# Kernel tuning notes

Hardware: AMD Instinct MI355X
Metric: run time of the kernel (lower is better)

## Reference

```python
import jax, jax.numpy as jnp
import numpy as np

BS, QLEN, KLEN = 2, 64, 64
N_HEADS, D_KV = 8, 64
INNER = N_HEADS * D_KV  # 512
VOCAB = 4096


def _layernorm(x, g, b, eps=1e-6):
    m = jnp.mean(x, axis=-1, keepdims=True)
    v = jnp.mean(jnp.square(x - m), axis=-1, keepdims=True)
    return (x - m) * jax.lax.rsqrt(v + eps) * g + b


def _l2norm(x, eps=1e-12):
    sq = jnp.sum(jnp.square(x), axis=-1, keepdims=True)
    return x * jax.lax.rsqrt(jnp.maximum(sq, eps))


def setup_inputs() -> dict:
    key = jax.random.key(0)
    ks = jax.random.split(key, 8)
    d = {
        'query': jax.random.normal(ks[0], (BS, QLEN, INNER), jnp.float32),
        'key': jax.random.normal(ks[1], (BS, KLEN, INNER), jnp.float32),
        'q_position_embeddings': jax.random.normal(ks[2], (BS, QLEN, INNER), jnp.float32),
        'k_position_embeddings': jax.random.normal(ks[3], (BS, KLEN, INNER), jnp.float32),
        'wi_w': jax.random.normal(ks[4], (2 * INNER, INNER), jnp.float32) / np.sqrt(2 * INNER),
        'vq_dict': jax.random.normal(ks[5], (VOCAB, D_KV), jnp.float32) * np.sqrt(2.0 / (VOCAB + D_KV)),
        'vq_ln_g': jnp.ones((D_KV,), jnp.float32),
        'vq_ln_b': jnp.zeros((D_KV,), jnp.float32),
        'vq_o_w': jax.random.normal(ks[6], (D_KV, D_KV), jnp.float32) / np.sqrt(D_KV),
        'ln_g': jnp.ones((D_KV,), jnp.float32),
        'ln_b': jnp.zeros((D_KV,), jnp.float32),
    }
    return d


def reference(query, key, q_position_embeddings, k_position_embeddings,
              wi_w, vq_dict, vq_ln_g, vq_ln_b, vq_o_w, ln_g, ln_b):
    bs, qlen, dim = query.shape
    klen = key.shape[1]

    q = query + q_position_embeddings
    k = key + k_position_embeddings
    # wi(concat([q, 0])) == q @ wi_w[:dim]; wi(concat([0, k])) == k @ wi_w[dim:]
    q_proj = jnp.einsum('bqd,de->bqe', q, wi_w[:dim])   # [bs, qlen, inner]
    k_proj = jnp.einsum('bkd,de->bke', k, wi_w[dim:])   # [bs, klen, inner]

    # pairwise outer sum -> [bs, qlen, klen, inner] -> tokens of size d_kv
    rcr = q_proj[:, :, None, :] + k_proj[:, None, :, :]
    y = rcr.reshape(bs, qlen * klen * N_HEADS, D_KV)

    # --- VectorQuantizer (eval mode: no dropout, loss = 0) ---
    y_n = _l2norm(y)
    d_n = _l2norm(vq_dict)
    sim = jnp.einsum('bnd,vd->bnv', y_n, d_n)           # [bs, N, vocab]
    word_idx = jnp.argmax(sim, axis=-1)                 # [bs, N] int
    word_sim = jnp.max(sim, axis=-1)                    # [bs, N]
    z = vq_dict[word_idx]                               # gather
    emb = jax.lax.stop_gradient(z - y) + y              # straight-through
    emb = _layernorm(emb, vq_ln_g, vq_ln_b)
    emb = jnp.einsum('bnd,de->bne', emb, vq_o_w)

    r3 = emb.reshape(bs, qlen, klen, N_HEADS, D_KV)
    r3_scores = word_sim.reshape(bs, qlen, klen, N_HEADS, 1)
    out_ids = word_idx.reshape(bs, qlen, klen, N_HEADS, 1)

    r3_weighted = jnp.mean(r3 * r3_scores, axis=2)      # [bs, qlen, n_heads, d_kv]
    r3_weighted = jnp.transpose(r3_weighted, (0, 2, 1, 3))  # [bs, n_heads, qlen, d_kv]
    r3_weighted = _layernorm(r3_weighted, ln_g, ln_b)
    return r3_weighted, out_ids, r3_scores
```

## Files before the change

### kernel.cpp

```cpp
#include <hip/hip_runtime.h>
#include <math.h>

#define BS 2
#define QLEN 64
#define KLEN 64
#define NH 8
#define DKV 64
#define INNER 512
#define VOCAB 4096
#define CHUNKV 64
#define RS 130
#define BUFD (CHUNKV * RS)

typedef double vdbl4 __attribute__((ext_vector_type(4)));
typedef double vdbl2 __attribute__((ext_vector_type(2)));


__global__ __launch_bounds__(256) void k_prep(
    const float* __restrict__ q_in, const float* __restrict__ k_in,
    const float* __restrict__ qpe, const float* __restrict__ kpe,
    const float* __restrict__ wi,
    const float* __restrict__ vq, const float* __restrict__ g,
    const float* __restrict__ bta, const float* __restrict__ ow,
    double* __restrict__ qp, double* __restrict__ kp,
    double* __restrict__ dnt, float* __restrict__ E,
    unsigned long long* __restrict__ bestf)
{
    __shared__ double S[1600];
    __shared__ float Osh[4096];
    int bid = blockIdx.x;
    int t = threadIdx.x;

    if (bid < 1024) {
        int side = bid >> 9;
        int b    = (bid >> 8) & 1;
        int rp   = (bid >> 3) & 31;
        int cb   = bid & 7;
        const float* xin = side ? k_in : q_in;
        const float* pin = side ? kpe : qpe;
        double* outp = side ? kp : qp;
        int wrow0 = side ? INNER : 0;
        int r0 = rp * 2;
        double* xs = S;
        double* red = S + 1024;
        for (int i = t; i < 2 * INNER; i += 256) {
            int rr = i >> 9, dd = i & 511;
            int gidx = (b * 64 + r0 + rr) * INNER + dd;
            xs[rr * INNER + dd] = (double)xin[gidx] + (double)pin[gidx];
        }
        __syncthreads();
        int col = cb * 64 + (t & 63);
        int dh = t >> 6;
        double a0 = 0.0, a1 = 0.0;
        #pragma unroll 8
        for (int d = dh * 128; d < dh * 128 + 128; ++d) {
            double w = (double)wi[(size_t)(wrow0 + d) * INNER + col];
            a0 = fma(xs[d], w, a0);
            a1 = fma(xs[INNER + d], w, a1);
        }
        red[(dh * 2 + 0) * 64 + (t & 63)] = a0;
        red[(dh * 2 + 1) * 64 + (t & 63)] = a1;
        __syncthreads();
        if (t < 128) {
            int rr = t >> 6, c2 = t & 63;
            double s = (red[(0 * 2 + rr) * 64 + c2] + red[(1 * 2 + rr) * 64 + c2])
                     + (red[(2 * 2 + rr) * 64 + c2] + red[(3 * 2 + rr) * 64 + c2]);
            outp[(size_t)(b * 64 + r0 + rr) * INNER + cb * 64 + c2] = s;
        }
    } else {
        int db = bid - 1024;
        if (db < 256) bestf[db * 256 + t] = 0ull;
        double* Lsh = S;
        double* Dsh = S + 256;
        int vb = db * 4;
        int wv = t >> 6, lane = t & 63;
        for (int i = t; i < 4096; i += 256) Osh[i] = ow[i];
        int v = vb + wv;
        double z = (double)vq[v * DKV + lane];
        double s2 = z * z, s1 = z;
        for (int m = 32; m >= 1; m >>= 1) { s2 += __shfl_xor(s2, m); s1 += __shfl_xor(s1, m); }
        Dsh[lane * 5 + wv] = z * (1.0 / sqrt(fmax(s2, 1e-12)));
        double mean = s1 * (1.0 / 64.0);
        double d0 = z - mean;
        double vv2 = d0 * d0;
        for (int m = 32; m >= 1; m >>= 1) vv2 += __shfl_xor(vv2, m);
        vv2 *= (1.0 / 64.0);
        Lsh[wv * 64 + lane] = d0 * (1.0 / sqrt(vv2 + 1e-6)) * (double)g[lane] + (double)bta[lane];
        __syncthreads();
        double c0 = 0.0, c1 = 0.0, c2 = 0.0, c3 = 0.0;
        #pragma unroll 4
        for (int gg = 0; gg < 16; ++gg) {
            int jj = gg * 4;
            c0 = fma(Lsh[wv * 64 + jj + 0], (double)Osh[(jj + 0) * 64 + lane], c0);
            c1 = fma(Lsh[wv * 64 + jj + 1], (double)Osh[(jj + 1) * 64 + lane], c1);
            c2 = fma(Lsh[wv * 64 + jj + 2], (double)Osh[(jj + 2) * 64 + lane], c2);
            c3 = fma(Lsh[wv * 64 + jj + 3], (double)Osh[(jj + 3) * 64 + lane], c3);
        }
        E[v * DKV + lane] = (float)((c0 + c1) + (c2 + c3));
        {
            int j = t >> 2, vloc = t & 3;
            dnt[(size_t)j * VOCAB + vb + vloc] = Dsh[j * 5 + vloc];
        }
    }
}

__global__ __launch_bounds__(1024, 4) void k_simscan(
    const double* __restrict__ qp, const double* __restrict__ kp,
    const double* __restrict__ dnt,
    unsigned long long* __restrict__ bestf)
{
    int bid = blockIdx.x;
    int bh = bid & 15, cg = bid >> 4;
    int b = bh >> 3, h = bh & 7;
    int t = threadIdx.x;
    int w = t >> 6, l = t & 63;

    __shared__ double S[2 * BUFD];
    __shared__ int sem[8];

    int asub = l >> 4;
    int lrow = l & 15;
    bool isprod = (w < 8);

    if (t < 8) sem[t] = 0;

    int drow[4], dcol[4];
    {
        vdbl4 prow = (vdbl4){0.0, 0.0, 0.0, 0.0};
        vdbl4 pcol = (vdbl4){0.0, 0.0, 0.0, 0.0};
        double a_row = (asub == 0) ? (double)lrow : 0.0;
        double b_one = (asub == 0) ? 1.0 : 0.0;
        double a_one = (asub == 0) ? 1.0 : 0.0;
        double b_col = (asub == 0) ? (double)lrow : 0.0;
        prow = __builtin_amdgcn_mfma_f64_16x16x4f64(a_row, b_one, prow, 0, 0, 0);
        pcol = __builtin_amdgcn_mfma_f64_16x16x4f64(a_one, b_col, pcol, 0, 0, 0);
        #pragma unroll
        for (int r = 0; r < 4; ++r) { drow[r] = (int)prow[r]; dcol[r] = (int)pcol[r]; }
    }

    double afr[16];
    if (isprod) {
        const double* src = (w < 4) ? qp : kp;
        int arow = (w & 3) * 16 + lrow;
        #pragma unroll
        for (int ks = 0; ks < 16; ++ks)
            afr[ks] = src[(size_t)(b * 64 + arow) * INNER + h * 64 + ks * 4 + asub];
    }

    int ci = t - 512;
    int qg = ci & 15, kg = (ci >> 4) & 31;
    double best[4][2];
    #pragma unroll
    for (int i = 0; i < 4; ++i)
        #pragma unroll
        for (int j = 0; j < 2; ++j) best[i][j] = 0.0;

    __syncthreads();

    if (isprod) {
        for (int step = 0; step < 4; ++step) {
            if (step >= 2) {
                for (;;) {
                    int c0 = 0;
                    if (l == 0) c0 = atomicAdd(&sem[4 + step - 2], 0);
                    if (__shfl(c0, 0) >= 8) break;
                    __builtin_amdgcn_s_sleep(2);
                }
            }
            int v0 = (cg * 4 + step) * CHUNKV;
            double* buf = S + (step & 1) * BUFD;
            vdbl4 acc[4];
            #pragma unroll
            for (int vt = 0; vt < 4; ++vt) acc[vt] = (vdbl4){0.0, 0.0, 0.0, 0.0};
            size_t base = (size_t)asub * VOCAB + v0 + lrow;
            double bcur[4], bnext[4];
            #pragma unroll
            for (int vt = 0; vt < 4; ++vt) bcur[vt] = dnt[base + vt * 16];
            #pragma unroll
            for (int ks = 0; ks < 16; ++ks) {
                if (ks < 15) {
                    size_t krow = base + (size_t)((ks + 1) * 4) * VOCAB;
                    #pragma unroll
                    for (int vt = 0; vt < 4; ++vt) bnext[vt] = dnt[krow + vt * 16];
                }
                #pragma unroll
                for (int vt = 0; vt < 4; ++vt)
                    acc[vt] = __builtin_amdgcn_mfma_f64_16x16x4f64(
                        afr[ks], bcur[vt], acc[vt], 0, 0, 0);
                if (ks < 15) {
                    #pragma unroll
                    for (int vt = 0; vt < 4; ++vt) bcur[vt] = bnext[vt];
                }
            }
            bool isq = (w < 4);
            #pragma unroll
            for (int vt = 0; vt < 4; ++vt)
                #pragma unroll
                for (int r = 0; r < 4; ++r) {
                    int vl = vt * 16 + dcol[r];
                    int grow = (w & 3) * 16 + drow[r];
                    int slot = isq ? ((grow & 15) * 4 + (grow >> 4))
                                   : (64 + (grow & 31) * 2 + (grow >> 5));
                    unsigned long long code =
                        (unsigned long long)((4095 - (v0 + vl)) << 1);
                    double s = fma(acc[vt][r], 1.0 / 64.0, 1.5);
                    unsigned long long bb2 = __double_as_longlong(s) & ~0x1FFFull;
                    if (isq) bb2 |= code;
                    buf[vl * RS + slot] = __longlong_as_double(bb2);
                }
            __threadfence_block();
            if (l == 0) atomicAdd(&sem[step], 1);
        }
    } else {
        for (int step = 0; step < 4; ++step) {
            for (;;) {
                int c0 = 0;
                if (l == 0) c0 = atomicAdd(&sem[step], 0);
                if (__shfl(c0, 0) >= 8) break;
                __builtin_amdgcn_s_sleep(2);
            }
            double* buf = S + (step & 1) * BUFD;
            #pragma unroll 2
            for (int v = 0; v < CHUNKV; ++v) {
                vdbl2 q01 = *(const vdbl2*)&buf[v * RS + qg * 4];
                vdbl2 q23 = *(const vdbl2*)&buf[v * RS + qg * 4 + 2];
                vdbl2 k01 = *(const vdbl2*)&buf[v * RS + 64 + kg * 2];
                best[0][0] = fmax(best[0][0], q01[0] + k01[0]);
                best[0][1] = fmax(best[0][1], q01[0] + k01[1]);
                best[1][0] = fmax(best[1][0], q01[1] + k01[0]);
                best[1][1] = fmax(best[1][1], q01[1] + k01[1]);
                best[2][0] = fmax(best[2][0], q23[0] + k01[0]);
                best[2][1] = fmax(best[2][1], q23[0] + k01[1]);
                best[3][0] = fmax(best[3][0], q23[1] + k01[0]);
                best[3][1] = fmax(best[3][1], q23[1] + k01[1]);
            }
            __threadfence_block();
            if (l == 0) atomicAdd(&sem[4 + step], 1);
        }
        #pragma unroll
        for (int i = 0; i < 4; ++i)
            #pragma unroll
            for (int j = 0; j < 2; ++j) {
                int q = qg + 16 * i, k = kg + 32 * j;
                atomicMax(&bestf[((size_t)bh * 64 + q) * 64 + k],
                          (unsigned long long)__double_as_longlong(best[i][j]));
            }
    }
}

__global__ __launch_bounds__(256) void k_combine(
    const unsigned long long* __restrict__ bestf,
    const double* __restrict__ qp, const double* __restrict__ kp,
    const float* __restrict__ E,
    const float* __restrict__ lng, const float* __restrict__ lnb,
    float* __restrict__ out)
{
    int bid = blockIdx.x;
    int bh = bid & 15, q = bid >> 4;
    int b = bh >> 3, h = bh & 7;
    int t = threadIdx.x;
    int w = t >> 6, lane = t & 63;

    __shared__ double qrow[64];
    __shared__ double gpart[4][64];
    __shared__ double knpart[4][64];
    __shared__ double qnpart[4];
    __shared__ float  ws_l[64];
    __shared__ int    idx_l[64];
    __shared__ float  epart[4][64];

    if (t < 64) qrow[t] = qp[(size_t)(b * 64 + q) * INNER + h * 64 + t];
    __syncthreads();

    {
        const double* krow = kp + (size_t)(b * 64 + lane) * INNER + h * 64 + w * 16;
        double gd = 0.0, kn = 0.0;
        #pragma unroll
        for (int i = 0; i < 16; ++i) {
            double xk = krow[i];
            gd = fma(qrow[w * 16 + i], xk, gd);
            kn = fma(xk, xk, kn);
        }
        gpart[w][lane] = gd;
        knpart[w][lane] = kn;
        if (lane == 0) {
            double qn = 0.0;
            #pragma unroll
            for (int i = 0; i < 16; ++i) { double xq = qrow[w * 16 + i]; qn = fma(xq, xq, qn); }
            qnpart[w] = qn;
        }
    }
    __syncthreads();

    if (w == 0) {
        int k = lane;
        double gdot = (gpart[0][k] + gpart[1][k]) + (gpart[2][k] + gpart[3][k]);
        double kn2  = (knpart[0][k] + knpart[1][k]) + (knpart[2][k] + knpart[3][k]);
        double qn2  = (qnpart[0] + qnpart[1]) + (qnpart[2] + qnpart[3]);
        unsigned long long bb = bestf[((size_t)bh * 64 + q) * 64 + k];
        int vidx = 4095 - (int)(bb & 0xFFFull);
        double sval = __longlong_as_double(bb & ~0x1FFFull);
        double tru = (sval - 3.0) * 64.0;
        double n2 = qn2 + kn2 + 2.0 * gdot;
        double wsim = tru * (1.0 / sqrt(fmax(n2, 1e-12)));
        size_t oidx = ((size_t)(b * QLEN + q) * KLEN + k) * NH + h;
        out[65536 + oidx] = (float)vidx;
        out[131072 + oidx] = (float)wsim;
        ws_l[k] = (float)wsim;
        idx_l[k] = vidx;
    }
    __syncthreads();

    {
        int d = lane;
        float acc = 0.0f;
        #pragma unroll 4
        for (int k2 = w * 16; k2 < w * 16 + 16; ++k2)
            acc += E[idx_l[k2] * DKV + d] * ws_l[k2];
        epart[w][d] = acc;
    }
    __syncthreads();

    if (w == 0) {
        int d = lane;
        float acc = ((epart[0][d] + epart[1][d]) + (epart[2][d] + epart[3][d])) * (1.0f / 64.0f);
        float mean = acc;
        for (int m = 32; m >= 1; m >>= 1) mean += __shfl_xor(mean, m);
        mean *= (1.0f / 64.0f);
        float dv = acc - mean;
        float var = dv * dv;
        for (int m = 32; m >= 1; m >>= 1) var += __shfl_xor(var, m);
        var *= (1.0f / 64.0f);
        float o = dv * rsqrtf(var + 1e-6f) * lng[d] + lnb[d];
        out[(((size_t)b * NH + h) * QLEN + q) * DKV + d] = o;
    }
}

extern "C" void kernel_launch(void* const* d_in, const int* in_sizes, int n_in,
                              void* d_out, int out_size, void* d_ws, size_t ws_size,
                              hipStream_t stream) {
    const float* query = (const float*)d_in[0];
    const float* key   = (const float*)d_in[1];
    const float* qpe   = (const float*)d_in[2];
    const float* kpe   = (const float*)d_in[3];
    const float* wi    = (const float*)d_in[4];
    const float* vq    = (const float*)d_in[5];
    const float* vqg   = (const float*)d_in[6];
    const float* vqb   = (const float*)d_in[7];
    const float* ow    = (const float*)d_in[8];
    const float* lng   = (const float*)d_in[9];
    const float* lnb   = (const float*)d_in[10];
    float* out = (float*)d_out;

    char* ws = (char*)d_ws;
    double* qp  = (double*)(ws + 0);
    double* kp  = (double*)(ws + 524288);
    double* dnt = (double*)(ws + 1048576);
    float*  E   = (float*) (ws + 3145728);
    unsigned long long* bestf = (unsigned long long*)(ws + 4194304);

    k_prep   <<<2048, 256, 0, stream>>>(query, key, qpe, kpe, wi, vq, vqg, vqb, ow,
                                        qp, kp, dnt, E, bestf);
    k_simscan<<<256, 1024, 0, stream>>>(qp, kp, dnt, bestf);
    k_combine<<<1024, 256, 0, stream>>>(bestf, qp, kp, E, lng, lnb, out);
}
```

Before: 153.5 us.

## Use FP64 MFMA for projection GEMM in prep kernel with larger tiles

Rewrites the q/k projection part of k_prep to use 16x16x4 FP64 MFMA instructions on 16-row tiles with a split-K reduction through shared memory, instead of scalar FMA over two rows per block. The dictionary-preparation branch is regrouped to handle 8 vocab entries per 512-thread block, and the launch shrinks from 2048 to 768 blocks. This cuts redundant weight reads and scalar FP64 work in the prep stage. The cost is a large shared-memory footprint (about 128 KB) that may limit occupancy, plus an MFMA trick used to derive the output lane layout.

```diff
diff --git a/kernel.cpp b/kernel.cpp
--- a/kernel.cpp
+++ b/kernel.cpp
@@ -11,12 +11,13 @@
 #define CHUNKV 64
 #define RS 130
 #define BUFD (CHUNKV * RS)
+#define XSTR 514
 
 typedef double vdbl4 __attribute__((ext_vector_type(4)));
 typedef double vdbl2 __attribute__((ext_vector_type(2)));
 
 
-__global__ __launch_bounds__(256) void k_prep(
+__global__ __launch_bounds__(512) void k_prep(
     const float* __restrict__ q_in, const float* __restrict__ k_in,
     const float* __restrict__ qpe, const float* __restrict__ kpe,
     const float* __restrict__ wi,
@@ -26,60 +27,93 @@
     double* __restrict__ dnt, float* __restrict__ E,
     unsigned long long* __restrict__ bestf)
 {
-    __shared__ double S[1600];
-    __shared__ float Osh[4096];
+    __shared__ double S[16448];
     int bid = blockIdx.x;
     int t = threadIdx.x;
-
-    if (bid < 1024) {
-        int side = bid >> 9;
-        int b    = (bid >> 8) & 1;
-        int rp   = (bid >> 3) & 31;
-        int cb   = bid & 7;
+    int w = t >> 6, l = t & 63;
+    int lrow = l & 15, asub = l >> 4;
+
+    if (bid < 256) {
+        int rt = bid >> 4, cg = bid & 15;
+        int side = rt >> 3;
         const float* xin = side ? k_in : q_in;
         const float* pin = side ? kpe : qpe;
         double* outp = side ? kp : qp;
         int wrow0 = side ? INNER : 0;
-        int r0 = rp * 2;
         double* xs = S;
-        double* red = S + 1024;
-        for (int i = t; i < 2 * INNER; i += 256) {
-            int rr = i >> 9, dd = i & 511;
-            int gidx = (b * 64 + r0 + rr) * INNER + dd;
-            xs[rr * INNER + dd] = (double)xin[gidx] + (double)pin[gidx];
+        double* red = S + 8224;
+
+        int drow[4], dcol[4];
+        {
+            vdbl4 prow = (vdbl4){0.0, 0.0, 0.0, 0.0};
+            vdbl4 pcol = (vdbl4){0.0, 0.0, 0.0, 0.0};
+            double a_row = (asub == 0) ? (double)lrow : 0.0;
+            double b_one = (asub == 0) ? 1.0 : 0.0;
+            double a_one = (asub == 0) ? 1.0 : 0.0;
+            double b_col = (asub == 0) ? (double)lrow : 0.0;
+            prow = __builtin_amdgcn_mfma_f64_16x16x4f64(a_row, b_one, prow, 0, 0, 0);
+            pcol = __builtin_amdgcn_mfma_f64_16x16x4f64(a_one, b_col, pcol, 0, 0, 0);
+            #pragma unroll
+            for (int r = 0; r < 4; ++r) { drow[r] = (int)prow[r]; dcol[r] = (int)pcol[r]; }
+        }
+
+        for (int i = t; i < 16 * 512; i += 512) {
+            int r = i >> 9, d = i & 511;
+            int grow = rt * 16 + r;
+            int b = (grow >> 6) & 1, row = grow & 63;
+            int gg = (b * 64 + row) * INNER + d;
+            xs[r * XSTR + d] = (double)xin[gg] + (double)pin[gg];
         }
         __syncthreads();
-        int col = cb * 64 + (t & 63);
-        int dh = t >> 6;
-        double a0 = 0.0, a1 = 0.0;
-        #pragma unroll 8
-        for (int d = dh * 128; d < dh * 128 + 128; ++d) {
-            double w = (double)wi[(size_t)(wrow0 + d) * INNER + col];
-            a0 = fma(xs[d], w, a0);
-            a1 = fma(xs[INNER + d], w, a1);
-        }
-        red[(dh * 2 + 0) * 64 + (t & 63)] = a0;
-        red[(dh * 2 + 1) * 64 + (t & 63)] = a1;
+
+        int cq = w & 1, kq = w >> 1;
+        int colb = cg * 32 + cq * 16;
+        int k0 = kq * 128;
+        vdbl4 acc = (vdbl4){0.0, 0.0, 0.0, 0.0};
+        double bf[2];
+        #pragma unroll
+        for (int p = 0; p < 2; ++p)
+            bf[p] = (double)wi[(size_t)(wrow0 + k0 + p * 4 + asub) * INNER + colb + lrow];
+        #pragma unroll 4
+        for (int ks = 0; ks < 32; ++ks) {
+            double a = xs[lrow * XSTR + k0 + ks * 4 + asub];
+            double bc = bf[ks & 1];
+            if (ks < 30)
+                bf[ks & 1] = (double)wi[(size_t)(wrow0 + k0 + (ks + 2) * 4 + asub) * INNER
+                                        + colb + lrow];
+            acc = __builtin_amdgcn_mfma_f64_16x16x4f64(a, bc, acc, 0, 0, 0);
+        }
+        {
+            double* rr = red + (size_t)(cq * 4 + kq) * 1028;
+            #pragma unroll
+            for (int r = 0; r < 4; ++r) rr[l * 4 + r] = acc[r];
+        }
         __syncthreads();
-        if (t < 128) {
-            int rr = t >> 6, c2 = t & 63;
-            double s = (red[(0 * 2 + rr) * 64 + c2] + red[(1 * 2 + rr) * 64 + c2])
-                     + (red[(2 * 2 + rr) * 64 + c2] + red[(3 * 2 + rr) * 64 + c2]);
-            outp[(size_t)(b * 64 + r0 + rr) * INNER + cb * 64 + c2] = s;
+        if (kq == 0) {
+            #pragma unroll
+            for (int r = 0; r < 4; ++r) {
+                int base = l * 4 + r;
+                double s0 = red[(cq * 4 + 0) * 1028 + base] + red[(cq * 4 + 1) * 1028 + base];
+                double s1 = red[(cq * 4 + 2) * 1028 + base] + red[(cq * 4 + 3) * 1028 + base];
+                int grow = rt * 16 + drow[r];
+                int b = (grow >> 6) & 1, row = grow & 63;
+                outp[(size_t)(b * 64 + row) * INNER + colb + dcol[r]] = s0 + s1;
+            }
         }
     } else {
-        int db = bid - 1024;
-        if (db < 256) bestf[db * 256 + t] = 0ull;
+        int db = bid - 256;
+        if (t < 128) bestf[db * 128 + t] = 0ull;
         double* Lsh = S;
-        double* Dsh = S + 256;
-        int vb = db * 4;
-        int wv = t >> 6, lane = t & 63;
-        for (int i = t; i < 4096; i += 256) Osh[i] = ow[i];
+        double* Dsh = S + 512;
+        float*  Osh = (float*)(S + 1088);
+        int vb = db * 8;
+        int wv = w, lane = l;
+        for (int i = t; i < 4096; i += 512) Osh[i] = ow[i];
         int v = vb + wv;
         double z = (double)vq[v * DKV + lane];
         double s2 = z * z, s1 = z;
         for (int m = 32; m >= 1; m >>= 1) { s2 += __shfl_xor(s2, m); s1 += __shfl_xor(s1, m); }
-        Dsh[lane * 5 + wv] = z * (1.0 / sqrt(fmax(s2, 1e-12)));
+        Dsh[lane * 9 + wv] = z * (1.0 / sqrt(fmax(s2, 1e-12)));
         double mean = s1 * (1.0 / 64.0);
         double d0 = z - mean;
         double vv2 = d0 * d0;
@@ -98,8 +132,8 @@
         }
         E[v * DKV + lane] = (float)((c0 + c1) + (c2 + c3));
         {
-            int j = t >> 2, vloc = t & 3;
-            dnt[(size_t)j * VOCAB + vb + vloc] = Dsh[j * 5 + vloc];
+            int j = t >> 3, vloc = t & 7;
+            dnt[(size_t)j * VOCAB + vb + vloc] = Dsh[j * 9 + vloc];
         }
     }
 }
@@ -359,8 +393,8 @@
     float*  E   = (float*) (ws + 3145728);
     unsigned long long* bestf = (unsigned long long*)(ws + 4194304);
 
-    k_prep   <<<2048, 256, 0, stream>>>(query, key, qpe, kpe, wi, vq, vqg, vqb, ow,
-                                        qp, kp, dnt, E, bestf);
+    k_prep   <<<768, 512, 0, stream>>>(query, key, qpe, kpe, wi, vq, vqg, vqb, ow,
+                                       qp, kp, dnt, E, bestf);
     k_simscan<<<256, 1024, 0, stream>>>(qp, kp, dnt, bestf);
     k_combine<<<1024, 256, 0, stream>>>(bestf, qp, kp, E, lng, lnb, out);
 }
```

Measured after the change: 157.7 us. +2.7%, slower.
